# Optimization experiments

Hardware: AMD Instinct MI355X
Metric: run time of the kernel (lower is better)

The kernel has to match this reference:

```python
import jax, jax.numpy as jnp
import numpy as np

B, N, E1, H, D = 16, 256, 4, 8, 128  # batch, max nodes, edge types+1, heads, dim
VOCAB = 100


def setup_inputs() -> dict:
    key = jax.random.key(0)
    ks = jax.random.split(key, 20)
    s = 0.05
    return dict(
        node_feat=jax.random.randint(ks[0], (B, N), 0, VOCAB),
        L=jax.random.normal(ks[1], (B, N, N, E1), jnp.float32),
        emb=jax.random.normal(ks[2], (VOCAB, D), jnp.float32) * s,
        W0=jax.random.normal(ks[3], (E1, H, D, D), jnp.float32) * s,
        W1=jax.random.normal(ks[4], (E1, H, D * H * E1, D), jnp.float32) * (s / 4.0),
        a1w0=jax.random.normal(ks[5], (E1, H, D), jnp.float32) * s,
        a1b0=jnp.zeros((E1, H), jnp.float32),
        a2w0=jax.random.normal(ks[6], (E1, H, D), jnp.float32) * s,
        a2b0=jnp.zeros((E1, H), jnp.float32),
        a1w1=jax.random.normal(ks[7], (E1, H, D), jnp.float32) * s,
        a1b1=jnp.zeros((E1, H), jnp.float32),
        a2w1=jax.random.normal(ks[8], (E1, H, D), jnp.float32) * s,
        a2b1=jnp.zeros((E1, H), jnp.float32),
        sb0=jnp.zeros((E1, H, D), jnp.float32),
        sb1=jnp.zeros((E1, H, D), jnp.float32),
        outW=jax.random.normal(ks[9], (D, D), jnp.float32) * s,
        outb=jnp.zeros((D,), jnp.float32),
        attW=jax.random.normal(ks[10], (D,), jnp.float32) * s,
        attb=jnp.zeros((), jnp.float32),
    )


def _gat_layer(state, Ltr, W, a1w, a1b, a2w, a2b, sb, last):
    # state: (B, N, Din); W: (E1, H, Din, D); Ltr: (E1, 1, B, N, N)
    Wh = jnp.einsum('bni,ehio->ehbno', state, W)                      # (E1,H,B,N,D)
    s1 = jnp.einsum('ehbno,eho->ehbn', Wh, a1w) + a1b[:, :, None, None]
    s2 = jnp.einsum('ehbno,eho->ehbn', Wh, a2w) + a2b[:, :, None, None]
    logits = jax.nn.leaky_relu(s1[..., :, None] + s2[..., None, :], 0.2) + Ltr
    att = jax.nn.softmax(logits, axis=3)  # torch softmax over dim=1 of (B,N,N)
    h = jnp.einsum('ehbnm,ehbmo->ehbno', att, Wh) + sb[:, :, None, None, :]
    if last:
        return jnp.mean(h, axis=(0, 1))                               # (B,N,D)
    h = jax.nn.elu(h)
    # concat order in torch: outer edge-type jj, inner head ii -> (B,N,E1*H*D)
    return jnp.transpose(h, (2, 3, 0, 1, 4)).reshape(state.shape[0], state.shape[1], -1)


def reference(node_feat, L, emb, W0, W1, a1w0, a1b0, a2w0, a2b0,
              a1w1, a1b1, a2w1, a2b1, sb0, sb1, outW, outb, attW, attb):
    Ltr = jnp.transpose(L, (3, 0, 1, 2))[:, None]  # (E1,1,B,N,N)
    state = emb[node_feat]                         # (B,N,D)
    state = _gat_layer(state, Ltr, W0, a1w0, a1b0, a2w0, a2b0, sb0, last=False)
    state = _gat_layer(state, Ltr, W1, a1w1, a1b1, a2w1, a2b1, sb1, last=True)
    y = state @ outW + outb                        # (B,N,D)
    aw = jax.nn.sigmoid(state @ attW + attb)       # (B,N)
    y = aw[..., None] * y
    return jnp.mean(y, axis=1)                     # (B,D)
```

## Files before the change

### kernel.cpp

```cpp
#include <hip/hip_runtime.h>
#include <hip/hip_bf16.h>

#define Bq 16
#define Nq 256
#define E1q 4
#define Hq 8
#define Dq 128
#define EH 32
#define BN 4096

typedef __hip_bfloat16 bf16;
typedef short bf16x8 __attribute__((ext_vector_type(8)));
typedef float f32x4 __attribute__((ext_vector_type(4)));

__device__ __forceinline__ void gll16(const void* gptr, void* lptr) {
    __builtin_amdgcn_global_load_lds(
        (const __attribute__((address_space(1))) void*)gptr,
        (__attribute__((address_space(3))) void*)lptr, 16, 0, 0);
}

__device__ __forceinline__ unsigned short f2bf(float v) {
    __hip_bfloat16 h = __float2bfloat16(v);
    return *(unsigned short*)&h;
}

__device__ __forceinline__ void transpose_tile(const float* __restrict__ W,
                                               bf16* __restrict__ WT, int K,
                                               int kt, int nt, int eh,
                                               float (*tile)[65], int tid) {
    int tr = tid >> 6, tc = tid & 63;
    const float* src = W + ((size_t)eh * K + kt * 64) * 128 + nt * 64;
#pragma unroll
    for (int p = 0; p < 16; ++p) {
        int r = p * 4 + tr;
        tile[r][tc] = src[(size_t)r * 128 + tc];
    }
    __syncthreads();
    bf16* dst = WT + ((size_t)eh * 128 + nt * 64) * K + kt * 64;
#pragma unroll
    for (int p = 0; p < 16; ++p) {
        int n = p * 4 + tr;
        dst[(size_t)n * K + tc] = __float2bfloat16(tile[tc][n]);
    }
}

__global__ __launch_bounds__(256) void prep_kernel(const int* __restrict__ nf,
                                                   const float* __restrict__ emb,
                                                   const float* __restrict__ W0,
                                                   const float* __restrict__ W1,
                                                   const float* __restrict__ L,
                                                   bf16* __restrict__ st0b,
                                                   bf16* __restrict__ W0T,
                                                   bf16* __restrict__ W1T,
                                                   float* __restrict__ Le) {
    int bid = blockIdx.x;
    int t = threadIdx.x;
    __shared__ float tile[64][65];
    if (bid < 2048) {
        int i = bid * 256 + t;
        int row = i >> 7, col = i & 127;
        st0b[i] = __float2bfloat16(emb[nf[row] * Dq + col]);
    } else if (bid < 2176) {
        int id2 = bid - 2048;
        transpose_tile(W0, W0T, 128, id2 & 1, (id2 >> 1) & 1, id2 >> 2, tile, t);
    } else if (bid < 6272) {
        int id3 = bid - 2176;
        transpose_tile(W1, W1T, 4096, id3 & 63, (id3 >> 6) & 1, id3 >> 7, tile, t);
    } else {
        int idx = (bid - 6272) * 256 + t;
        float4 v = *(const float4*)(L + (size_t)idx * 4);
        Le[idx] = v.x;
        Le[1048576 + idx] = v.y;
        Le[2097152 + idx] = v.z;
        Le[3145728 + idx] = v.w;
    }
}

__global__ __launch_bounds__(256) void mfma_gemm_kernel(const bf16* __restrict__ Ab,
                                                        const bf16* __restrict__ Bt,
                                                        bf16* __restrict__ Wht,
                                                        const float* __restrict__ a1w,
                                                        const float* __restrict__ a1b,
                                                        const float* __restrict__ a2w,
                                                        const float* __restrict__ a2b,
                                                        float* __restrict__ s1,
                                                        float* __restrict__ s2, int K) {
    int id = blockIdx.x;
    int xcd = id & 7, slot = id >> 3;
    int eh = (slot & 3) * 8 + xcd;
    int rt = slot >> 2;
    int tid = threadIdx.x;
    int w = tid >> 6, l = tid & 63;
    int q = l >> 4, mn = l & 15;
    __shared__ __align__(16) bf16 As[128 * 64];
    __shared__ __align__(16) bf16 Bs[128 * 64];
    __shared__ float red1[128], red2[128];
    const bf16* Ap = Ab + (size_t)(rt * 128) * K;
    const bf16* Bp = Bt + (size_t)eh * 128 * K;
    int lr = l >> 3;
    int g = (l & 7) ^ lr;
    int gcol = g * 8;

    if (tid < 128) { red1[tid] = 0.f; red2[tid] = 0.f; }

    f32x4 acc[4][4];
#pragma unroll
    for (int i = 0; i < 4; i++)
#pragma unroll
        for (int j = 0; j < 4; j++) acc[i][j] = (f32x4){0.f, 0.f, 0.f, 0.f};

    int wr = (w >> 1) * 64, wc = (w & 1) * 64;
    int msw = mn & 7;

    for (int k0 = 0; k0 < K; k0 += 64) {
#pragma unroll
        for (int u = 0; u < 4; ++u) {
            int i = w * 4 + u;
            int r = i * 8 + lr;
            gll16(Ap + (size_t)r * K + k0 + gcol, (char*)As + i * 1024);
            gll16(Bp + (size_t)r * K + k0 + gcol, (char*)Bs + i * 1024);
        }
        __syncthreads();
#pragma unroll
        for (int kk = 0; kk < 2; ++kk) {
            int qb = ((kk * 4 + q) ^ msw) * 16;
            bf16x8 af[4], bfr[4];
#pragma unroll
            for (int i = 0; i < 4; ++i) {
                af[i]  = *(const bf16x8*)((const char*)As + (wr + i * 16 + mn) * 128 + qb);
                bfr[i] = *(const bf16x8*)((const char*)Bs + (wc + i * 16 + mn) * 128 + qb);
            }
#pragma unroll
            for (int i = 0; i < 4; ++i)
#pragma unroll
                for (int j = 0; j < 4; ++j)
                    acc[i][j] = __builtin_amdgcn_mfma_f32_16x16x32_bf16(af[i], bfr[j], acc[i][j], 0, 0, 0);
        }
        __syncthreads();
    }
#pragma unroll
    for (int i = 0; i < 4; ++i) {
        int r0 = rt * 128 + wr + i * 16 + q * 4;
        int b = r0 >> 8, m = r0 & 255;
#pragma unroll
        for (int j = 0; j < 4; ++j) {
            int o = wc + j * 16 + mn;
            ushort4 pk;
            pk.x = f2bf(acc[i][j][0]);
            pk.y = f2bf(acc[i][j][1]);
            pk.z = f2bf(acc[i][j][2]);
            pk.w = f2bf(acc[i][j][3]);
            *(ushort4*)(Wht + ((((size_t)eh * 16 + b) * 128 + o) * 256 + m)) = pk;
        }
    }
    float w1v[4], w2v[4];
#pragma unroll
    for (int j = 0; j < 4; ++j) {
        int o = wc + j * 16 + mn;
        w1v[j] = a1w[eh * 128 + o];
        w2v[j] = a2w[eh * 128 + o];
    }
#pragma unroll
    for (int i = 0; i < 4; ++i)
#pragma unroll
        for (int r = 0; r < 4; ++r) {
            float p1 = 0.f, p2 = 0.f;
#pragma unroll
            for (int j = 0; j < 4; ++j) {
                p1 += acc[i][j][r] * w1v[j];
                p2 += acc[i][j][r] * w2v[j];
            }
#pragma unroll
            for (int off = 1; off < 16; off <<= 1) {
                p1 += __shfl_xor(p1, off);
                p2 += __shfl_xor(p2, off);
            }
            if (mn == 0) {
                int row = wr + i * 16 + q * 4 + r;
                atomicAdd(&red1[row], p1);
                atomicAdd(&red2[row], p2);
            }
        }
    __syncthreads();
    if (tid < 128) {
        int rg = rt * 128 + tid;
        s1[eh * 4096 + rg] = red1[tid] + a1b[eh];
        s2[eh * 4096 + rg] = red2[tid] + a2b[eh];
    }
}

__global__ __launch_bounds__(256) void colsoft_kernel(const float* __restrict__ s1,
                                                      const float* __restrict__ s2,
                                                      const float* __restrict__ Le,
                                                      float4* __restrict__ stat) {
    int mt = blockIdx.x, b = blockIdx.y, e = blockIdx.z;
    int t = threadIdx.x;
    __shared__ float Lt[256 * 32];
    __shared__ float s1L[8 * 256];
#pragma unroll
    for (int i = 0; i < 8; ++i) s1L[i * 256 + t] = s1[(e * 8 + i) * 4096 + b * 256 + t];
    const float* Lb = Le + ((size_t)(e * 16 + b) * 256) * 256 + mt * 32;
#pragma unroll
    for (int j = 0; j < 8; ++j) {
        int f = t + 256 * j;
        int n = f >> 3, c4 = (f & 7) * 4;
        *(float4*)(Lt + n * 32 + c4) = *(const float4*)(Lb + (size_t)n * 256 + c4);
    }
    __syncthreads();
    int h = t >> 5, mm = t & 31;
    int m = mt * 32 + mm;
    float s2v = s2[(e * 8 + h) * 4096 + b * 256 + m];
    const float* s1p = s1L + h * 256;
    float s1max = -1e30f;
#pragma unroll
    for (int u = 0; u < 8; ++u) s1max = fmaxf(s1max, s1p[mm * 8 + u]);
#pragma unroll
    for (int off = 16; off; off >>= 1) s1max = fmaxf(s1max, __shfl_xor(s1max, off));
    float sm = s1max + s2v;
    float bound = (sm > 0.f ? sm : 0.2f * sm) + 8.0f;
    float sum = 0.f;
    for (int n = 0; n < 256; ++n) {
        float x = s1p[n] + s2v;
        x = x > 0.f ? x : 0.2f * x;
        x += Lt[n * 32 + mm];
        sum += __expf(x - bound);
    }
    float4 st = {s2v, bound, 1.0f / sum, 0.f};
    stat[(e * 8 + h) * 4096 + b * 256 + m] = st;
}

template <int LAST>
__global__ __launch_bounds__(256) void att_mfma_kernel(const float* __restrict__ s1,
                                                       const float4* __restrict__ stat,
                                                       const float* __restrict__ Le,
                                                       const bf16* __restrict__ Wht,
                                                       const float* __restrict__ sb,
                                                       bf16* __restrict__ outb) {
    int nt = blockIdx.x;
    int b = blockIdx.y;
    int eh = blockIdx.z;
    int e = eh >> 3;
    int tid = threadIdx.x;
    int w = tid >> 6, l = tid & 63;
    int q = l >> 4, mn = l & 15;
    __shared__ __align__(16) bf16 As[128 * 32];
    __shared__ __align__(16) bf16 Bs[128 * 40];
    __shared__ float s1L[128];
    __shared__ __align__(16) float4 stL[256];

    int base = eh * 4096 + b * 256;
    if (tid < 128) s1L[tid] = s1[base + nt * 128 + tid];
    stL[tid] = stat[base + tid];
    __syncthreads();

    const bf16* Whtp = Wht + ((size_t)eh * 16 + b) * 32768;
    int nl = tid >> 1, mh = (tid & 1) * 16;
    const float* Lrow = Le + (((size_t)(e * 16 + b) * 256) + nt * 128 + nl) * 256;
    float s1v = s1L[nl];
    int srow = l >> 2;
    int sq = (l & 3) ^ ((l >> 3) & 3);
    int scol = sq * 8;
    int rsw = ((mn >> 1) & 3) << 3;

    f32x4 acc[4][4];
#pragma unroll
    for (int i = 0; i < 4; i++)
#pragma unroll
        for (int j = 0; j < 4; j++) acc[i][j] = (f32x4){0.f, 0.f, 0.f, 0.f};

    int wr = (w >> 1) * 64, wc = (w & 1) * 64;

    float4 lv[4];
#pragma unroll
    for (int jj = 0; jj < 4; ++jj) lv[jj] = *(const float4*)(Lrow + mh + jj * 4);

    for (int k0 = 0; k0 < 256; k0 += 32) {
#pragma unroll
        for (int u = 0; u < 2; ++u) {
            int i = 2 * w + u;
            gll16(Whtp + (size_t)(i * 16 + srow) * 256 + k0 + scol, (char*)As + i * 1024);
        }
        float4 cur[4];
#pragma unroll
        for (int jj = 0; jj < 4; ++jj) cur[jj] = lv[jj];
        if (k0 + 32 < 256) {
#pragma unroll
            for (int jj = 0; jj < 4; ++jj)
                lv[jj] = *(const float4*)(Lrow + k0 + 32 + mh + jj * 4);
        }
#pragma unroll
        for (int jj = 0; jj < 4; ++jj) {
            int mb = mh + jj * 4;
            float av[4];
#pragma unroll
            for (int c = 0; c < 4; ++c) {
                int m = k0 + mb + c;
                float4 stv = stL[m];
                float x = s1v + stv.x;
                x = x > 0.f ? x : 0.2f * x;
                x += ((const float*)&cur[jj])[c];
                av[c] = __expf(x - stv.y) * stv.z;
            }
            unsigned int u01 = (unsigned int)f2bf(av[0]) | ((unsigned int)f2bf(av[1]) << 16);
            unsigned int u23 = (unsigned int)f2bf(av[2]) | ((unsigned int)f2bf(av[3]) << 16);
            unsigned int* bp = (unsigned int*)Bs + (nl * 40 + mb) / 2;
            bp[0] = u01;
            bp[1] = u23;
        }
        __syncthreads();
        bf16x8 af[4], bfr[4];
#pragma unroll
        for (int i = 0; i < 4; ++i) {
            af[i]  = *(const bf16x8*)(As + (wr + i * 16 + mn) * 32 + ((q << 3) ^ rsw));
            bfr[i] = *(const bf16x8*)(Bs + (wc + i * 16 + mn) * 40 + q * 8);
        }
#pragma unroll
        for (int i = 0; i < 4; ++i)
#pragma unroll
            for (int j = 0; j < 4; ++j)
                acc[i][j] = __builtin_amdgcn_mfma_f32_16x16x32_bf16(af[i], bfr[j], acc[i][j], 0, 0, 0);
        __syncthreads();
    }
#pragma unroll
    for (int i = 0; i < 4; ++i) {
        int o0 = wr + i * 16 + q * 4;
        float4 sbv = *(const float4*)(sb + eh * 128 + o0);
#pragma unroll
        for (int j = 0; j < 4; ++j) {
            int n = wc + j * 16 + mn;
            float v0 = acc[i][j][0] + sbv.x;
            float v1 = acc[i][j][1] + sbv.y;
            float v2 = acc[i][j][2] + sbv.z;
            float v3 = acc[i][j][3] + sbv.w;
            if (LAST == 0) {
                v0 = v0 > 0.f ? v0 : __expf(v0) - 1.f;
                v1 = v1 > 0.f ? v1 : __expf(v1) - 1.f;
                v2 = v2 > 0.f ? v2 : __expf(v2) - 1.f;
                v3 = v3 > 0.f ? v3 : __expf(v3) - 1.f;
                ushort4 pk = {f2bf(v0), f2bf(v1), f2bf(v2), f2bf(v3)};
                *(ushort4*)(outb + (size_t)(b * 256 + nt * 128 + n) * 4096 + eh * Dq + o0) = pk;
            } else {
                ushort4 pk = {f2bf(v0), f2bf(v1), f2bf(v2), f2bf(v3)};
                *(ushort4*)(outb + ((size_t)eh * 4096 + b * 256 + nt * 128 + n) * Dq + o0) = pk;
            }
        }
    }
}

__global__ __launch_bounds__(256) void reduce_aw_kernel(const bf16* __restrict__ h2b,
                                                        const float* __restrict__ attW,
                                                        const float* __restrict__ attb,
                                                        float* __restrict__ st2,
                                                        float* __restrict__ aw) {
    int t = threadIdx.x;
    int rl = t >> 7, o = t & 127;
    int r = blockIdx.x * 2 + rl;
    float acc = 0.f;
#pragma unroll
    for (int eh = 0; eh < EH; ++eh)
        acc += __bfloat162float(h2b[((size_t)eh * 4096 + r) * 128 + o]);
    acc *= (1.0f / 32.0f);
    st2[(size_t)r * 128 + o] = acc;
    float p = acc * attW[o];
#pragma unroll
    for (int off = 32; off; off >>= 1) p += __shfl_down(p, off);
    __shared__ float part[4];
    if ((t & 63) == 0) part[t >> 6] = p;
    __syncthreads();
    if (t == 0) aw[r] = 1.0f / (1.0f + __expf(-(part[0] + part[1] + attb[0])));
    if (t == 128) aw[r] = 1.0f / (1.0f + __expf(-(part[2] + part[3] + attb[0])));
}

__global__ __launch_bounds__(128) void final_kernel(const float* __restrict__ st2,
                                                    const float* __restrict__ aw,
                                                    const float* __restrict__ outW,
                                                    const float* __restrict__ outb,
                                                    float* __restrict__ out) {
    int b = blockIdx.x;
    int t = threadIdx.x;
    __shared__ float awL[256], zL[128];
    awL[t] = aw[b * 256 + t];
    awL[t + 128] = aw[b * 256 + t + 128];
    __syncthreads();
    float z = 0.f;
    for (int n = 0; n < 256; ++n) z += awL[n] * st2[(size_t)(b * 256 + n) * Dq + t];
    float sa = 0.f;
    for (int n = 0; n < 256; ++n) sa += awL[n];
    zL[t] = z;
    __syncthreads();
    float acc = sa * outb[t];
    for (int o = 0; o < Dq; ++o) acc += zL[o] * outW[o * Dq + t];
    out[b * Dq + t] = acc * (1.0f / 256.0f);
}

extern "C" void kernel_launch(void* const* d_in, const int* in_sizes, int n_in,
                              void* d_out, int out_size, void* d_ws, size_t ws_size,
                              hipStream_t stream) {
    const int* nf = (const int*)d_in[0];
    const float* L = (const float*)d_in[1];
    const float* emb = (const float*)d_in[2];
    const float* W0 = (const float*)d_in[3];
    const float* W1 = (const float*)d_in[4];
    const float* a1w0 = (const float*)d_in[5];
    const float* a1b0 = (const float*)d_in[6];
    const float* a2w0 = (const float*)d_in[7];
    const float* a2b0 = (const float*)d_in[8];
    const float* a1w1 = (const float*)d_in[9];
    const float* a1b1 = (const float*)d_in[10];
    const float* a2w1 = (const float*)d_in[11];
    const float* a2b1 = (const float*)d_in[12];
    const float* sb0 = (const float*)d_in[13];
    const float* sb1 = (const float*)d_in[14];
    const float* outW = (const float*)d_in[15];
    const float* outb = (const float*)d_in[16];
    const float* attW = (const float*)d_in[17];
    const float* attb = (const float*)d_in[18];

    char* p = (char*)d_ws;
    bf16* st0b = (bf16*)(p);
    bf16* W0T  = (bf16*)(p + 1048576);
    bf16* W1T  = (bf16*)(p + 2097152);
    bf16* st1b = (bf16*)(p + 35651584);
    bf16* h2b  = (bf16*)(p + 2097152);
    float* Le  = (float*)(p + 69206016);
    bf16* Wht  = (bf16*)(p + 85983232);
    float* s1  = (float*)(p + 119537664);
    float* s2  = (float*)(p + 120061952);
    float4* stat = (float4*)(p + 120586240);
    float* st2 = (float*)(p);
    float* aw  = s1;
    float* outp = (float*)d_out;

    prep_kernel<<<10368, 256, 0, stream>>>(nf, emb, W0, W1, L, st0b, W0T, W1T, Le);

    mfma_gemm_kernel<<<1024, 256, 0, stream>>>(st0b, W0T, Wht, a1w0, a1b0, a2w0, a2b0, s1, s2, 128);
    colsoft_kernel<<<dim3(8, 16, 4), 256, 0, stream>>>(s1, s2, Le, stat);
    att_mfma_kernel<0><<<dim3(2, 16, 32), 256, 0, stream>>>(s1, stat, Le, Wht, sb0, st1b);

    mfma_gemm_kernel<<<1024, 256, 0, stream>>>(st1b, W1T, Wht, a1w1, a1b1, a2w1, a2b1, s1, s2, 4096);
    colsoft_kernel<<<dim3(8, 16, 4), 256, 0, stream>>>(s1, s2, Le, stat);
    att_mfma_kernel<1><<<dim3(2, 16, 32), 256, 0, stream>>>(s1, stat, Le, Wht, sb1, h2b);

    reduce_aw_kernel<<<2048, 256, 0, stream>>>(h2b, attW, attb, st2, aw);
    final_kernel<<<16, 128, 0, stream>>>(st2, aw, outW, outb, outp);
}
```

Before: 465.5 us.

## Add 256x256-tile pipelined MFMA GEMM for the layer-1 K=4096 projection

Replaces the generic MFMA GEMM for the second layer's large-K projection with a dedicated kernel that uses 256x256 tiles, 512 threads, and a 4-stage global_load_lds ring buffer with split A/B staging interleaved between MFMA halves. The kernel also remaps blocks to XCD-friendly order and fuses the attention score dot products into the epilogue, covering two heads per tile. The goal is higher arithmetic intensity and hiding load latency on the dominant GEMM. In exchange it uses 128KB of LDS and 256 blocks, which limits occupancy and relies on hand-tuned waitcnt sequencing.

```diff
diff --git a/kernel.cpp b/kernel.cpp
--- a/kernel.cpp
+++ b/kernel.cpp
@@ -189,6 +189,164 @@
     }
 }
 
+__global__ __launch_bounds__(512, 2) void gemm4k_kernel(const bf16* __restrict__ Ab,
+                                                        const bf16* __restrict__ Bt,
+                                                        bf16* __restrict__ Wht,
+                                                        const float* __restrict__ a1w,
+                                                        const float* __restrict__ a1b,
+                                                        const float* __restrict__ a2w,
+                                                        const float* __restrict__ a2b,
+                                                        float* __restrict__ s1,
+                                                        float* __restrict__ s2) {
+    __shared__ __align__(16) char smem[131072];
+    int bid = blockIdx.x;
+    int wg = (bid & 7) * 32 + (bid >> 3);
+    int tm = wg >> 4, tn = wg & 15;
+    int tid = threadIdx.x;
+    int wid = tid >> 6, l = tid & 63;
+    int wr = wid >> 2, wc = wid & 3;
+    int lhi = l >> 4, llo = l & 15;
+    int sa = (lhi ^ ((l >> 1) & 3)) << 4;
+    int skq = (l & 3) ^ ((l >> 3) & 3);
+
+    const bf16* Ap = Ab + (size_t)tm * 256 * 4096;
+    const bf16* Bp = Bt + (size_t)tn * 256 * 4096;
+    const bf16* sA = Ap + (size_t)(wid * 16 + (l >> 2)) * 4096 + skq * 8;
+    const bf16* sB = Bp + (size_t)(wid * 16 + (l >> 2)) * 4096 + skq * 8;
+    char* dA = (char*)smem + wid * 1024;
+    char* dB = (char*)smem + 65536 + wid * 1024;
+
+    auto stageA = [&](int tt) {
+        int bo = (tt & 3) * 16384;
+        gll16(sA + tt * 32, dA + bo);
+        gll16(sA + (size_t)128 * 4096 + tt * 32, dA + bo + 8192);
+    };
+    auto stageB = [&](int tt) {
+        int bo = (tt & 3) * 16384;
+        gll16(sB + tt * 32, dB + bo);
+        gll16(sB + (size_t)128 * 4096 + tt * 32, dB + bo + 8192);
+    };
+
+    f32x4 acc[8][4];
+#pragma unroll
+    for (int i = 0; i < 8; ++i)
+#pragma unroll
+        for (int j = 0; j < 4; ++j) acc[i][j] = (f32x4){0.f, 0.f, 0.f, 0.f};
+
+    int aoff = ((wr * 64 + llo) << 6) + sa;
+    int boff[4];
+#pragma unroll
+    for (int n = 0; n < 4; ++n)
+        boff[n] = 65536 + (((n >> 1) * 128 + wc * 32 + (n & 1) * 16 + llo) << 6) + sa;
+
+    stageA(0); stageB(0); stageA(1); stageB(1); stageA(2); stageB(2);
+    asm volatile("s_waitcnt vmcnt(8)" ::: "memory");
+    __builtin_amdgcn_s_barrier();
+
+#pragma unroll 1
+    for (int t = 0; t < 128; ++t) {
+        int bo = (t & 3) * 16384;
+        const char* sm = (const char*)smem;
+        bf16x8 af[4], bv[4];
+#pragma unroll
+        for (int m = 0; m < 4; ++m)
+            af[m] = *(const bf16x8*)(sm + bo + aoff + m * 1024);
+#pragma unroll
+        for (int n = 0; n < 4; ++n)
+            bv[n] = *(const bf16x8*)(sm + bo + boff[n]);
+        if (t < 125) stageA(t + 3);
+        __builtin_amdgcn_s_barrier();
+        asm volatile("s_waitcnt lgkmcnt(0)" ::: "memory");
+        __builtin_amdgcn_sched_barrier(0);
+        __builtin_amdgcn_s_setprio(1);
+#pragma unroll
+        for (int m = 0; m < 4; ++m)
+#pragma unroll
+            for (int n = 0; n < 4; ++n)
+                acc[m][n] = __builtin_amdgcn_mfma_f32_16x16x32_bf16(af[m], bv[n], acc[m][n], 0, 0, 0);
+        __builtin_amdgcn_s_setprio(0);
+        __builtin_amdgcn_s_barrier();
+#pragma unroll
+        for (int m = 0; m < 4; ++m)
+            af[m] = *(const bf16x8*)(sm + bo + aoff + 8192 + m * 1024);
+        if (t < 125) {
+            stageB(t + 3);
+            asm volatile("s_waitcnt vmcnt(8)" ::: "memory");
+        } else if (t == 125) {
+            asm volatile("s_waitcnt vmcnt(4)" ::: "memory");
+        } else if (t == 126) {
+            asm volatile("s_waitcnt vmcnt(0)" ::: "memory");
+        }
+        __builtin_amdgcn_s_barrier();
+        asm volatile("s_waitcnt lgkmcnt(0)" ::: "memory");
+        __builtin_amdgcn_sched_barrier(0);
+        __builtin_amdgcn_s_setprio(1);
+#pragma unroll
+        for (int m = 0; m < 4; ++m)
+#pragma unroll
+            for (int n = 0; n < 4; ++n)
+                acc[4 + m][n] = __builtin_amdgcn_mfma_f32_16x16x32_bf16(af[m], bv[n], acc[4 + m][n], 0, 0, 0);
+        __builtin_amdgcn_s_setprio(0);
+        __builtin_amdgcn_s_barrier();
+    }
+
+    float* red = (float*)smem;
+    red[tid] = 0.f;
+    red[tid + 512] = 0.f;
+    float w1v[4], w2v[4];
+#pragma unroll
+    for (int n = 0; n < 4; ++n) {
+        int eh = tn * 2 + (n >> 1);
+        int o = wc * 32 + (n & 1) * 16 + llo;
+        w1v[n] = a1w[eh * 128 + o];
+        w2v[n] = a2w[eh * 128 + o];
+    }
+    __syncthreads();
+#pragma unroll
+    for (int mi = 0; mi < 8; ++mi) {
+        int R = (mi >> 2) * 128 + wr * 64 + (mi & 3) * 16 + lhi * 4;
+#pragma unroll
+        for (int n = 0; n < 4; ++n) {
+            int eh = tn * 2 + (n >> 1);
+            int o = wc * 32 + (n & 1) * 16 + llo;
+            ushort4 pk;
+            pk.x = f2bf(acc[mi][n][0]);
+            pk.y = f2bf(acc[mi][n][1]);
+            pk.z = f2bf(acc[mi][n][2]);
+            pk.w = f2bf(acc[mi][n][3]);
+            *(ushort4*)(Wht + ((((size_t)eh * 16 + tm) * 128 + o) * 256 + R)) = pk;
+        }
+#pragma unroll
+        for (int r = 0; r < 4; ++r) {
+            float p10 = acc[mi][0][r] * w1v[0] + acc[mi][1][r] * w1v[1];
+            float p11 = acc[mi][2][r] * w1v[2] + acc[mi][3][r] * w1v[3];
+            float p20 = acc[mi][0][r] * w2v[0] + acc[mi][1][r] * w2v[1];
+            float p21 = acc[mi][2][r] * w2v[2] + acc[mi][3][r] * w2v[3];
+#pragma unroll
+            for (int off = 1; off < 16; off <<= 1) {
+                p10 += __shfl_xor(p10, off);
+                p11 += __shfl_xor(p11, off);
+                p20 += __shfl_xor(p20, off);
+                p21 += __shfl_xor(p21, off);
+            }
+            if (llo == 0) {
+                int row = R + r;
+                atomicAdd(&red[row], p10);
+                atomicAdd(&red[256 + row], p11);
+                atomicAdd(&red[512 + row], p20);
+                atomicAdd(&red[768 + row], p21);
+            }
+        }
+    }
+    __syncthreads();
+    {
+        int ehl = tid >> 8, row = tid & 255;
+        int eh = tn * 2 + ehl;
+        s1[eh * 4096 + tm * 256 + row] = red[ehl * 256 + row] + a1b[eh];
+        s2[eh * 4096 + tm * 256 + row] = red[512 + ehl * 256 + row] + a2b[eh];
+    }
+}
+
 __global__ __launch_bounds__(256) void colsoft_kernel(const float* __restrict__ s1,
                                                       const float* __restrict__ s2,
                                                       const float* __restrict__ Le,
@@ -437,7 +595,7 @@
     colsoft_kernel<<<dim3(8, 16, 4), 256, 0, stream>>>(s1, s2, Le, stat);
     att_mfma_kernel<0><<<dim3(2, 16, 32), 256, 0, stream>>>(s1, stat, Le, Wht, sb0, st1b);
 
-    mfma_gemm_kernel<<<1024, 256, 0, stream>>>(st1b, W1T, Wht, a1w1, a1b1, a2w1, a2b1, s1, s2, 4096);
+    gemm4k_kernel<<<256, 512, 0, stream>>>(st1b, W1T, Wht, a1w1, a1b1, a2w1, a2b1, s1, s2);
     colsoft_kernel<<<dim3(8, 16, 4), 256, 0, stream>>>(s1, s2, Le, stat);
     att_mfma_kernel<1><<<dim3(2, 16, 32), 256, 0, stream>>>(s1, stat, Le, Wht, sb1, h2b);
 
```

Result: faster. 421.6 us (-9.4%).
